# Kernel optimization log

Measured on AMD Instinct MI355X. Metric: run time of the kernel, lower is better.

The kernel has to match this reference:

```python
import jax, jax.numpy as jnp
import numpy as np

VOCAB_SIZE = 256
CODEC_VOCAB = 1024  # 2 ** codec_bits
D = 1024
NHEAD = 16
FF = 4096
L = 6
ENROLLED = 225  # enrolled_codec_sec(3) * codec_rate(75)
B, TT, TA = 4, 128, 512


def sinusoidal_pe(T, d):
    pos = np.arange(T, dtype=np.float32)[:, None]
    div = np.exp(np.arange(0, d, 2, dtype=np.float32) * (-np.log(10000.0) / d))
    pe = np.zeros((T, d), dtype=np.float32)
    pe[:, 0::2] = np.sin(pos * div)
    pe[:, 1::2] = np.cos(pos * div)
    return jnp.asarray(pe)


def layernorm(x, w, b, eps=1e-5):
    mu = x.mean(-1, keepdims=True)
    var = ((x - mu) ** 2).mean(-1, keepdims=True)
    return (x - mu) * jax.lax.rsqrt(var + eps) * w + b


def mha(q_in, kv_in, in_w, in_b, out_w, out_b, mask=None):
    # q_in: [B,Tq,D], kv_in: [B,Tk,D]; mask True == blocked (torch attn_mask convention)
    d = q_in.shape[-1]
    h, hd = NHEAD, d // NHEAD
    wq, wk, wv = in_w[:d], in_w[d:2 * d], in_w[2 * d:]
    bq, bk, bv = in_b[:d], in_b[d:2 * d], in_b[2 * d:]
    Bq, Tq, _ = q_in.shape
    Tk = kv_in.shape[1]
    q = (q_in @ wq.T + bq).reshape(Bq, Tq, h, hd)
    k = (kv_in @ wk.T + bk).reshape(Bq, Tk, h, hd)
    v = (kv_in @ wv.T + bv).reshape(Bq, Tk, h, hd)
    scores = jnp.einsum('bqhd,bkhd->bhqk', q, k) / jnp.sqrt(jnp.float32(hd))
    if mask is not None:
        scores = jnp.where(mask, -jnp.inf, scores)
    attn = jax.nn.softmax(scores, axis=-1)
    o = jnp.einsum('bhqk,bkhd->bqhd', attn, v).reshape(Bq, Tq, d)
    return o @ out_w.T + out_b


def pack(te, ae, ee, tl, al):
    # Ragged concat [text[:tl]; audio[:al]; enrolled] padded to static max_len.
    Tt, Ta, Te = te.shape[0], ae.shape[0], ee.shape[0]
    pos = jnp.arange(Tt + Ta + Te)
    t = te[jnp.clip(pos, 0, Tt - 1)]
    a = ae[jnp.clip(pos - tl, 0, Ta - 1)]
    e = ee[jnp.clip(pos - tl - al, 0, Te - 1)]
    x = jnp.where((pos < tl)[:, None], t,
        jnp.where((pos < tl + al)[:, None], a,
        jnp.where((pos < tl + al + Te)[:, None], e, jnp.zeros_like(t))))
    return x


def setup_inputs():
    key = jax.random.key(0)
    ks = iter(jax.random.split(key, 64))

    def n(shape, s=0.02):
        return jax.random.normal(next(ks), shape, dtype=jnp.float32) * s

    text = jax.random.randint(next(ks), (B, TT), 0, VOCAB_SIZE)
    audio = jax.random.randint(next(ks), (B, TA), 0, CODEC_VOCAB)
    enrolled_audio = jax.random.randint(next(ks), (B, ENROLLED), 0, CODEC_VOCAB)
    # force sample 0 to full length so max_len is static (= TT+TA+ENROLLED)
    text_len_batch = jax.random.randint(next(ks), (B,), TT // 2, TT + 1).at[0].set(TT)
    audio_len_batch = jax.random.randint(next(ks), (B,), TA // 2, TA + 1).at[0].set(TA)
    return dict(
        text=text, audio=audio, enrolled_audio=enrolled_audio,
        text_len_batch=text_len_batch, audio_len_batch=audio_len_batch,
        text_emb=n((VOCAB_SIZE, D)), audio_emb=n((CODEC_VOCAB, D)),
        sa_in_w=n((L, 3 * D, D)), sa_in_b=jnp.zeros((L, 3 * D), jnp.float32),
        sa_out_w=n((L, D, D)), sa_out_b=jnp.zeros((L, D), jnp.float32),
        ca_in_w=n((L, 3 * D, D)), ca_in_b=jnp.zeros((L, 3 * D), jnp.float32),
        ca_out_w=n((L, D, D)), ca_out_b=jnp.zeros((L, D), jnp.float32),
        ff1_w=n((L, FF, D)), ff1_b=jnp.zeros((L, FF), jnp.float32),
        ff2_w=n((L, D, FF)), ff2_b=jnp.zeros((L, D), jnp.float32),
        ln1_w=jnp.ones((L, D), jnp.float32), ln1_b=jnp.zeros((L, D), jnp.float32),
        ln2_w=jnp.ones((L, D), jnp.float32), ln2_b=jnp.zeros((L, D), jnp.float32),
        ln3_w=jnp.ones((L, D), jnp.float32), ln3_b=jnp.zeros((L, D), jnp.float32),
        out_w=n((CODEC_VOCAB, D)), out_b=jnp.zeros((CODEC_VOCAB,), jnp.float32))


def reference(text, audio, enrolled_audio, text_len_batch, audio_len_batch,
              text_emb, audio_emb, sa_in_w, sa_in_b, sa_out_w, sa_out_b,
              ca_in_w, ca_in_b, ca_out_w, ca_out_b, ff1_w, ff1_b, ff2_w, ff2_b,
              ln1_w, ln1_b, ln2_w, ln2_b, ln3_w, ln3_b, out_w, out_b):
    # per-segment sinusoidal PE (positions reset at the start of each segment)
    te = text_emb[text] + sinusoidal_pe(text.shape[1], D)
    ae = audio_emb[audio] + sinusoidal_pe(audio.shape[1], D)
    ee = audio_emb[enrolled_audio] + sinusoidal_pe(enrolled_audio.shape[1], D)
    embed = jax.vmap(pack)(te, ae, ee, text_len_batch, audio_len_batch)  # [B, max_len, D]
    max_len = embed.shape[1]
    prefix = text.shape[1] + audio.shape[1]  # == max(tl+al) by construction
    mask = jnp.triu(jnp.ones((max_len, max_len), bool), 1).at[:, :prefix].set(False)
    mem = embed  # TransformerDecoder memory == embed
    x = embed
    for l in range(L):  # post-norm decoder layers (torch default norm_first=False)
        x = layernorm(x + mha(x, x, sa_in_w[l], sa_in_b[l], sa_out_w[l], sa_out_b[l], mask), ln1_w[l], ln1_b[l])
        x = layernorm(x + mha(x, mem, ca_in_w[l], ca_in_b[l], ca_out_w[l], ca_out_b[l]), ln2_w[l], ln2_b[l])
        h = jax.nn.relu(x @ ff1_w[l].T + ff1_b[l]) @ ff2_w[l].T + ff2_b[l]
        x = layernorm(x + h, ln3_w[l], ln3_b[l])
    return x @ out_w.T + out_b  # [B, max_len, CODEC_VOCAB]
```

## Files before the change

### kernel.cpp

```cpp
#include <hip/hip_runtime.h>
#include <hip/hip_bf16.h>

#define B_      4
#define TT_     128
#define TA_     512
#define TE_     225
#define T_      865
#define D_      1024
#define H_      16
#define FF_     4096
#define L_      6
#define PREFIX_ 640
#define M_TOK   (B_ * T_)
#define M_PAD   3584
#define NKV     (L_ * 2 * D_)

typedef __attribute__((ext_vector_type(8))) short          s16x8;
typedef __attribute__((ext_vector_type(4))) float          f32x4;
typedef __attribute__((ext_vector_type(8))) unsigned short u16x8;

typedef __attribute__((address_space(1))) const void gv_t;
typedef __attribute__((address_space(3))) void       lv_t;

__device__ __forceinline__ float bf2f(unsigned short u) {
  union { unsigned int i; float f; } c; c.i = ((unsigned int)u) << 16; return c.f;
}
__device__ __forceinline__ unsigned short f2bf(float f) {
  union { __hip_bfloat16 h; unsigned short u; } c; c.h = __float2bfloat16(f); return c.u;
}
template <int N> __device__ __forceinline__ void vmwait() {
  asm volatile("s_waitcnt vmcnt(%0)" :: "n"(N) : "memory");
}

__global__ __launch_bounds__(256) void embed_kernel(
    const int* __restrict__ text, const int* __restrict__ audio,
    const int* __restrict__ enrolled, const int* __restrict__ tl_b,
    const int* __restrict__ al_b, const float* __restrict__ text_emb,
    const float* __restrict__ audio_emb,
    float* __restrict__ xf, unsigned short* __restrict__ xb,
    unsigned short* __restrict__ memb, unsigned short* __restrict__ attnb) {
  int row = blockIdx.x;
  int d0 = threadIdx.x * 4;
  size_t off = (size_t)row * D_ + d0;
  if (row >= M_TOK) {
    *(unsigned long long*)&xb[off]    = 0ull;
    *(unsigned long long*)&memb[off]  = 0ull;
    *(unsigned long long*)&attnb[off] = 0ull;
    return;
  }
  int b = row / T_, pos = row - b * T_;
  int tl = tl_b[b], al = al_b[b];
  const float* emb = nullptr;
  int p = 0;
  if (pos < tl) {
    emb = text_emb + (size_t)text[b * TT_ + pos] * D_;
    p = pos;
  } else if (pos < tl + al) {
    emb = audio_emb + (size_t)audio[b * TA_ + (pos - tl)] * D_;
    p = pos - tl;
  } else if (pos < tl + al + TE_) {
    emb = audio_emb + (size_t)enrolled[b * TE_ + (pos - tl - al)] * D_;
    p = pos - tl - al;
  }
  float4 v;
  float* pv = (float*)&v;
  if (emb) {
    const float c = -9.2103403719761836f / (float)D_;
    #pragma unroll
    for (int e = 0; e < 4; ++e) {
      int d = d0 + e;
      int i = d >> 1;
      float freq = expf(c * (float)(2 * i));
      float arg = (float)p * freq;
      float pe = (d & 1) ? cosf(arg) : sinf(arg);
      pv[e] = emb[d] + pe;
    }
  } else {
    v = make_float4(0.f, 0.f, 0.f, 0.f);
  }
  *(float4*)&xf[off] = v;
  unsigned long long pk = (unsigned long long)f2bf(pv[0])
      | ((unsigned long long)f2bf(pv[1]) << 16)
      | ((unsigned long long)f2bf(pv[2]) << 32)
      | ((unsigned long long)f2bf(pv[3]) << 48);
  *(unsigned long long*)&xb[off]   = pk;
  *(unsigned long long*)&memb[off] = pk;
}

__global__ __launch_bounds__(256) void cvt_kernel(
    const float* __restrict__ in, unsigned short* __restrict__ out, int n8) {
  int i = blockIdx.x * 256 + threadIdx.x;
  if (i >= n8) return;
  const float4* pp = (const float4*)in + (size_t)i * 2;
  float4 a = pp[0], bq = pp[1];
  u16x8 o;
  o[0] = f2bf(a.x);  o[1] = f2bf(a.y);  o[2] = f2bf(a.z);  o[3] = f2bf(a.w);
  o[4] = f2bf(bq.x); o[5] = f2bf(bq.y); o[6] = f2bf(bq.z); o[7] = f2bf(bq.w);
  *(u16x8*)(out + (size_t)i * 8) = o;
}

__global__ __launch_bounds__(256) void cvt_layer_kernel(
    const float* __restrict__ s0, const float* __restrict__ s1,
    const float* __restrict__ s2, const float* __restrict__ s3,
    const float* __restrict__ s4, const float* __restrict__ s5,
    unsigned short* __restrict__ dst) {
  size_t e = ((size_t)blockIdx.x * 256 + threadIdx.x) * 8;
  if (e >= 16777216u) return;
  const float* src; size_t off;
  if      (e <  3145728u) { src = s0; off = e; }
  else if (e <  4194304u) { src = s1; off = e -  3145728u; }
  else if (e <  7340032u) { src = s2; off = e -  4194304u; }
  else if (e <  8388608u) { src = s3; off = e -  7340032u; }
  else if (e < 12582912u) { src = s4; off = e -  8388608u; }
  else                    { src = s5; off = e - 12582912u; }
  const float4* pp = (const float4*)(src + off);
  float4 a = pp[0], bq = pp[1];
  u16x8 o;
  o[0] = f2bf(a.x);  o[1] = f2bf(a.y);  o[2] = f2bf(a.z);  o[3] = f2bf(a.w);
  o[4] = f2bf(bq.x); o[5] = f2bf(bq.y); o[6] = f2bf(bq.z); o[7] = f2bf(bq.w);
  *(u16x8*)(dst + e) = o;
}

__global__ __launch_bounds__(256) void cvt_ckv_w(
    const float* __restrict__ ca_in_w, unsigned short* __restrict__ wckv) {
  int rr = blockIdx.x;
  int l = rr / (2 * D_), w = rr % (2 * D_);
  const float* src = ca_in_w + (size_t)l * 3 * D_ * D_ + (size_t)(D_ + w) * D_;
  unsigned short* dst = wckv + (size_t)rr * D_;
  int c = threadIdx.x * 4;
  float4 v4 = *(const float4*)(src + c);
  unsigned long long pk = (unsigned long long)f2bf(v4.x)
      | ((unsigned long long)f2bf(v4.y) << 16)
      | ((unsigned long long)f2bf(v4.z) << 32)
      | ((unsigned long long)f2bf(v4.w) << 48);
  *(unsigned long long*)&dst[c] = pk;
}

__global__ __launch_bounds__(256) void cvt_ckv_b(
    const float* __restrict__ ca_in_b, float* __restrict__ cbias) {
  int rr = blockIdx.x * 256 + threadIdx.x;
  if (rr >= NKV) return;
  int l = rr / (2 * D_), w = rr % (2 * D_);
  cbias[rr] = ca_in_b[(size_t)l * 3 * D_ + D_ + w];
}

template <int ACT, int OBF, int NSTRIPE>
__global__ __launch_bounds__(512, 2) void gemm_8w(
    const unsigned short* __restrict__ A, int lda,
    const unsigned short* __restrict__ W, int ldw,
    const float* __restrict__ bias,
    float* __restrict__ Cf, unsigned short* __restrict__ Cb, int ldc,
    int Mw, int K) {
  __shared__ unsigned short lds[2][2][256 * 64];
  int tid = threadIdx.x, lane = tid & 63, wid = tid >> 6;

  int gx = gridDim.x;
  int nwg = gx * gridDim.y;
  int orig = blockIdx.y * gx + blockIdx.x;
  int m0, n0;
  if (NSTRIPE && (gx & 7) == 0) {
    int stripe = gx >> 3;
    int xcd = orig & 7, loc = orig >> 3;
    n0 = (xcd * stripe + loc % stripe) * 256;
    m0 = (loc / stripe) * 256;
  } else {
    int q = nwg >> 3, r = nwg & 7;
    int xcd = orig & 7, loc = orig >> 3;
    int wg = (xcd < r ? xcd * (q + 1) : r * (q + 1) + (xcd - r) * q) + loc;
    m0 = (wg / gx) * 256;
    n0 = (wg % gx) * 256;
  }

  int wr = wid >> 2, wc = wid & 3;
  int r16 = lane & 15, g4 = lane >> 4;

  int srow = lane >> 3;
  int sgrp = (lane & 7) ^ srow;
  const unsigned short* gA[4];
  const unsigned short* gB[4];
  unsigned soff[4];
  #pragma unroll
  for (int c = 0; c < 4; ++c) {
    int rb = wid * 32 + c * 8;
    gA[c] = A + (size_t)(m0 + rb + srow) * lda + sgrp * 8;
    gB[c] = W + (size_t)(n0 + rb + srow) * ldw + sgrp * 8;
    soff[c] = rb * 64;
  }

  f32x4 acc[8][4];
  #pragma unroll
  for (int i = 0; i < 8; ++i)
    #pragma unroll
    for (int j = 0; j < 4; ++j) acc[i][j] = (f32x4)0.f;

  auto STAGE = [&](int bi, int t) {
    int k0 = t * 64;
    #pragma unroll
    for (int c = 0; c < 4; ++c)
      __builtin_amdgcn_global_load_lds((gv_t*)(gA[c] + k0),
          (lv_t*)&lds[bi][0][soff[c]], 16, 0, 0);
    #pragma unroll
    for (int c = 0; c < 4; ++c)
      __builtin_amdgcn_global_load_lds((gv_t*)(gB[c] + k0),
          (lv_t*)&lds[bi][1][soff[c]], 16, 0, 0);
  };

  STAGE(0, 0);
  int nt = K / 64, cur = 0;
  for (int t = 0; t < nt; ++t) {
    vmwait<0>();
    __builtin_amdgcn_s_barrier();
    if (t + 1 < nt) STAGE(cur ^ 1, t + 1);

    const unsigned short* Ab = &lds[cur][0][0];
    const unsigned short* Bb = &lds[cur][1][0];

    s16x8 bf_[4][2];
    #pragma unroll
    for (int j = 0; j < 4; ++j)
      #pragma unroll
      for (int kk = 0; kk < 2; ++kk) {
        int row = wc * 64 + j * 16 + r16;
        bf_[j][kk] = *(const s16x8*)&Bb[row * 64 + (((kk * 4 + g4) ^ (row & 7)) * 8)];
      }

    #pragma unroll
    for (int p = 0; p < 4; ++p) {
      s16x8 af_[2][2];
      #pragma unroll
      for (int ii = 0; ii < 2; ++ii)
        #pragma unroll
        for (int kk = 0; kk < 2; ++kk) {
          int row = wr * 128 + (p * 2 + ii) * 16 + r16;
          af_[ii][kk] = *(const s16x8*)&Ab[row * 64 + (((kk * 4 + g4) ^ (row & 7)) * 8)];
        }
      __builtin_amdgcn_s_setprio(1);
      #pragma unroll
      for (int kk = 0; kk < 2; ++kk)
        #pragma unroll
        for (int ii = 0; ii < 2; ++ii)
          #pragma unroll
          for (int j = 0; j < 4; ++j)
            acc[p * 2 + ii][j] = __builtin_amdgcn_mfma_f32_16x16x32_bf16(
                af_[ii][kk], bf_[j][kk], acc[p * 2 + ii][j], 0, 0, 0);
      __builtin_amdgcn_s_setprio(0);
    }
    cur ^= 1;
  }

  float bv[4];
  #pragma unroll
  for (int j = 0; j < 4; ++j) bv[j] = bias[n0 + wc * 64 + j * 16 + r16];
  int rbase = m0 + wr * 128 + g4 * 4;
  int cbase = n0 + wc * 64 + r16;
  #pragma unroll
  for (int i = 0; i < 8; ++i)
    #pragma unroll
    for (int rr = 0; rr < 4; ++rr) {
      int m = rbase + i * 16 + rr;
      if (m < Mw) {
        #pragma unroll
        for (int j = 0; j < 4; ++j) {
          float v = acc[i][j][rr] + bv[j];
          if (ACT) v = fmaxf(v, 0.f);
          if (OBF) Cb[(size_t)m * ldc + cbase + j * 16] = f2bf(v);
          else     Cf[(size_t)m * ldc + cbase + j * 16] = v;
        }
      }
    }
}

template <int BM, int BN, int BK, int ACT, int OBF, int NSTRIPE>
__global__ __launch_bounds__(256) void gemm_p2(
    const unsigned short* __restrict__ A, int lda,
    const unsigned short* __restrict__ W, int ldw,
    const float* __restrict__ bias,
    float* __restrict__ Cf, unsigned short* __restrict__ Cb, int ldc,
    int Mw, int K) {
  constexpr int WROWS = BM / 2, WCOLS = BN / 2;
  constexpr int WM = WROWS / 16, WN = WCOLS / 16;
  constexpr int LPR = BK / 8;
  constexpr int RPI = 64 / LPR;
  constexpr int ACH = (BM / 4) / RPI;
  constexpr int BCH = (BN / 4) / RPI;
  constexpr int ABUF = BM * BK, BBUF = BN * BK;
  constexpr int KSUB = BK / 32;
  constexpr int LW = ACH + BCH;
  __shared__ unsigned short lds[3 * (ABUF + BBUF)];

  int tid = threadIdx.x, lane = tid & 63, wid = tid >> 6;
  int gx = gridDim.x;
  int nwg = gx * gridDim.y;
  int orig = blockIdx.y * gx + blockIdx.x;
  int m0, n0;
  if (NSTRIPE && (gx & 7) == 0) {
    int stripe = gx >> 3;
    int xcd = orig & 7, loc = orig >> 3;
    n0 = (xcd * stripe + loc % stripe) * BN;
    m0 = (loc / stripe) * BM;
  } else {
    int q = nwg >> 3, r = nwg & 7;
    int xcd = orig & 7, loc = orig >> 3;
    int wg = (xcd < r ? xcd * (q + 1) : r * (q + 1) + (xcd - r) * q) + loc;
    m0 = (wg / gx) * BM;
    n0 = (wg % gx) * BN;
  }

  int wr = wid >> 1, wc = wid & 1;
  int lrow = lane / LPR, lgrp = lane % LPR;
  int skey = (BK == 32) ? ((lrow >> 1) & 3) : (lrow & 7);
  int lk = (lgrp ^ skey) * 8;

  const unsigned short* gAp[ACH]; unsigned aoff[ACH];
  const unsigned short* gBp[BCH]; unsigned boff[BCH];
  #pragma unroll
  for (int c = 0; c < ACH; ++c) {
    int row0 = wid * (BM / 4) + c * RPI;
    gAp[c] = A + (size_t)(m0 + row0 + lrow) * lda + lk;
    aoff[c] = row0 * BK;
  }
  #pragma unroll
  for (int c = 0; c < BCH; ++c) {
    int row0 = wid * (BN / 4) + c * RPI;
    gBp[c] = W + (size_t)(n0 + row0 + lrow) * ldw + lk;
    boff[c] = row0 * BK;
  }

  f32x4 acc[WM][WN];
  #pragma unroll
  for (int i = 0; i < WM; ++i)
    #pragma unroll
    for (int j = 0; j < WN; ++j) acc[i][j] = (f32x4)0.f;

  int frow = lane & 15, g4 = lane >> 4;

  auto STAGE = [&](int bi, int t) {
    int k0 = t * BK;
    #pragma unroll
    for (int c = 0; c < ACH; ++c)
      __builtin_amdgcn_global_load_lds((gv_t*)(gAp[c] + k0),
          (lv_t*)&lds[bi * ABUF + aoff[c]], 16, 0, 0);
    #pragma unroll
    for (int c = 0; c < BCH; ++c)
      __builtin_amdgcn_global_load_lds((gv_t*)(gBp[c] + k0),
          (lv_t*)&lds[3 * ABUF + bi * BBUF + boff[c]], 16, 0, 0);
  };

  STAGE(0, 0);
  STAGE(1, 1);
  int nt = K / BK;
  int cur = 0;
  for (int t = 0; t < nt; ++t) {
    if (t + 1 < nt) vmwait<LW>(); else vmwait<0>();
    __builtin_amdgcn_s_barrier();
    if (t + 2 < nt) {
      int stb = cur + 2; if (stb >= 3) stb -= 3;
      STAGE(stb, t + 2);
    }
    const unsigned short* Ab = &lds[cur * ABUF];
    const unsigned short* Bb = &lds[3 * ABUF + cur * BBUF];
    #pragma unroll
    for (int kk = 0; kk < KSUB; ++kk) {
      int rk = (BK == 32) ? ((g4 ^ ((frow >> 1) & 3)) * 8)
                          : (((kk * 4 + g4) ^ (frow & 7)) * 8);
      s16x8 af[WM], bfr[WN];
      #pragma unroll
      for (int i = 0; i < WM; ++i)
        af[i] = *(const s16x8*)&Ab[(wr * WROWS + i * 16 + frow) * BK + rk];
      #pragma unroll
      for (int j = 0; j < WN; ++j)
        bfr[j] = *(const s16x8*)&Bb[(wc * WCOLS + j * 16 + frow) * BK + rk];
      __builtin_amdgcn_s_setprio(1);
      #pragma unroll
      for (int i = 0; i < WM; ++i)
        #pragma unroll
        for (int j = 0; j < WN; ++j)
          acc[i][j] = __builtin_amdgcn_mfma_f32_16x16x32_bf16(af[i], bfr[j], acc[i][j], 0, 0, 0);
      __builtin_amdgcn_s_setprio(0);
    }
    cur = (cur == 2) ? 0 : cur + 1;
  }

  float bv[WN];
  #pragma unroll
  for (int j = 0; j < WN; ++j) bv[j] = bias[n0 + wc * WCOLS + j * 16 + (lane & 15)];
  int rbase = m0 + wr * WROWS + (lane >> 4) * 4;
  int cbase = n0 + wc * WCOLS + (lane & 15);
  #pragma unroll
  for (int i = 0; i < WM; ++i)
    #pragma unroll
    for (int rr = 0; rr < 4; ++rr) {
      int m = rbase + i * 16 + rr;
      if (m < Mw) {
        #pragma unroll
        for (int j = 0; j < WN; ++j) {
          float v = acc[i][j][rr] + bv[j];
          if (ACT) v = fmaxf(v, 0.f);
          if (OBF) Cb[(size_t)m * ldc + cbase + j * 16] = f2bf(v);
          else     Cf[(size_t)m * ldc + cbase + j * 16] = v;
        }
      }
    }
}

template <bool MASKED>
__global__ __launch_bounds__(256) void attn_mfma(
    const unsigned short* __restrict__ qp, int qld,
    const unsigned short* __restrict__ kp,
    const unsigned short* __restrict__ vp, int kvld,
    unsigned short* __restrict__ out) {
  __shared__ unsigned short KsL[64 * 64];
  __shared__ unsigned short VtL[64 * 72];
  __shared__ unsigned short PsL[4][16 * 64];
  int tid = threadIdx.x;
  int lane = tid & 63, wid = tid >> 6;
  int b = blockIdx.y >> 4, h = blockIdx.y & 15;
  int q0 = blockIdx.x * 64;
  int r16 = lane & 15, g4 = lane >> 4;

  int qrow = q0 + wid * 16 + r16;
  if (qrow >= T_) qrow = T_ - 1;
  const unsigned short* qbase =
      qp + (size_t)(b * T_ + qrow) * qld + h * 64 + g4 * 8;
  s16x8 qf0 = *(const s16x8*)qbase;
  s16x8 qf1 = *(const s16x8*)(qbase + 32);

  float m_[4], l_[4];
  f32x4 o_[4];
  #pragma unroll
  for (int rg = 0; rg < 4; ++rg) { m_[rg] = -INFINITY; l_[rg] = 0.f; }
  #pragma unroll
  for (int dj = 0; dj < 4; ++dj) o_[dj] = (f32x4)0.f;

  const int nt = MASKED ? max(10, (int)blockIdx.x + 1) : 14;

  for (int t = 0; t < nt; ++t) {
    int k0 = t * 64;
    __syncthreads();

    #pragma unroll
    for (int c = 0; c < 2; ++c) {
      int row = wid * 16 + c * 8 + (lane >> 3);
      int kr = k0 + row; if (kr >= T_) kr = T_ - 1;
      int grp = (lane & 7) ^ (row & 7);
      const unsigned short* src =
          kp + (size_t)(b * T_ + kr) * kvld + h * 64 + grp * 8;
      __builtin_amdgcn_global_load_lds((gv_t*)src,
          (lv_t*)&KsL[(wid * 16 + c * 8) * 64], 16, 0, 0);
    }
    {
      int vkr = k0 + lane; if (vkr >= T_) vkr = T_ - 1;
      const unsigned short* vsrc =
          vp + (size_t)(b * T_ + vkr) * kvld + h * 64 + wid * 16;
      u16x8 v0 = *(const u16x8*)vsrc;
      u16x8 v1 = *(const u16x8*)(vsrc + 8);
      #pragma unroll
      for (int jj = 0; jj < 8; ++jj) {
        VtL[(wid * 16 + jj) * 72 + lane]     = v0[jj];
        VtL[(wid * 16 + 8 + jj) * 72 + lane] = v1[jj];
      }
    }
    __syncthreads();

    f32x4 sj[4];
    #pragma unroll
    for (int j = 0; j < 4; ++j) sj[j] = (f32x4)0.f;
    __builtin_amdgcn_s_setprio(1);
    #pragma unroll
    for (int j = 0; j < 4; ++j) {
      int krow = j * 16 + r16;
      s16x8 kf0 = *(const s16x8*)&KsL[krow * 64 + ((g4 ^ (krow & 7)) * 8)];
      s16x8 kf1 = *(const s16x8*)&KsL[krow * 64 + (((4 + g4) ^ (krow & 7)) * 8)];
      sj[j] = __builtin_amdgcn_mfma_f32_16x16x32_bf16(qf0, kf0, sj[j], 0, 0, 0);
      sj[j] = __builtin_amdgcn_mfma_f32_16x16x32_bf16(qf1, kf1, sj[j], 0, 0, 0);
    }
    __builtin_amdgcn_s_setprio(0);

    float alpha_[4];
    #pragma unroll
    for (int rg = 0; rg < 4; ++rg) {
      int qa = q0 + wid * 16 + g4 * 4 + rg;
      float pm = -INFINITY;
      #pragma unroll
      for (int j = 0; j < 4; ++j) {
        int kg = k0 + j * 16 + r16;
        float sv = sj[j][rg] * 0.125f;
        bool bad = (kg >= T_) || (MASKED && kg > qa && kg >= PREFIX_);
        sv = bad ? -INFINITY : sv;
        sj[j][rg] = sv;
        pm = fmaxf(pm, sv);
      }
      pm = fmaxf(pm, __shfl_xor(pm, 1));
      pm = fmaxf(pm, __shfl_xor(pm, 2));
      pm = fmaxf(pm, __shfl_xor(pm, 4));
      pm = fmaxf(pm, __shfl_xor(pm, 8));
      float mn = fmaxf(m_[rg], pm);
      float al = __expf(m_[rg] - mn);
      m_[rg] = mn;
      alpha_[rg] = al;
      int prow = g4 * 4 + rg;
      float ps = 0.f;
      #pragma unroll
      for (int j = 0; j < 4; ++j) {
        float pv = __expf(sj[j][rg] - mn);
        ps += pv;
        PsL[wid][prow * 64 + (((j * 2 + (r16 >> 3)) ^ (prow & 7)) * 8) + (r16 & 7)]
            = f2bf(pv);
      }
      ps += __shfl_xor(ps, 1);
      ps += __shfl_xor(ps, 2);
      ps += __shfl_xor(ps, 4);
      ps += __shfl_xor(ps, 8);
      l_[rg] = l_[rg] * al + ps;
    }
    #pragma unroll
    for (int dj = 0; dj < 4; ++dj)
      #pragma unroll
      for (int rg = 0; rg < 4; ++rg) o_[dj][rg] *= alpha_[rg];

    __builtin_amdgcn_s_setprio(1);
    #pragma unroll
    for (int kk = 0; kk < 2; ++kk) {
      s16x8 pf = *(const s16x8*)
          &PsL[wid][r16 * 64 + (((kk * 4 + g4) ^ (r16 & 7)) * 8)];
      #pragma unroll
      for (int dj = 0; dj < 4; ++dj) {
        s16x8 vf = *(const s16x8*)
            &VtL[(dj * 16 + r16) * 72 + kk * 32 + g4 * 8];
        o_[dj] = __builtin_amdgcn_mfma_f32_16x16x32_bf16(pf, vf, o_[dj], 0, 0, 0);
      }
    }
    __builtin_amdgcn_s_setprio(0);
  }

  #pragma unroll
  for (int rg = 0; rg < 4; ++rg) {
    int qa = q0 + wid * 16 + g4 * 4 + rg;
    if (qa < T_) {
      float inv = 1.f / l_[rg];
      unsigned short* ob = out + (size_t)(b * T_ + qa) * D_ + h * 64;
      #pragma unroll
      for (int dj = 0; dj < 4; ++dj)
        ob[dj * 16 + r16] = f2bf(o_[dj][rg] * inv);
    }
  }
}

__global__ __launch_bounds__(256) void ln_res_kernel(
    float* __restrict__ x, const float* __restrict__ r,
    const float* __restrict__ w, const float* __restrict__ b,
    unsigned short* __restrict__ xb) {
  __shared__ float red[4];
  int row = blockIdx.x, tid = threadIdx.x;
  size_t off = (size_t)row * D_ + tid * 4;
  float4 xv = *(float4*)&x[off];
  float4 rv = *(const float4*)&r[off];
  float v0 = xv.x + rv.x, v1 = xv.y + rv.y, v2 = xv.z + rv.z, v3 = xv.w + rv.w;

  float s = v0 + v1 + v2 + v3;
  #pragma unroll
  for (int o = 1; o < 64; o <<= 1) s += __shfl_xor(s, o);
  if ((tid & 63) == 0) red[tid >> 6] = s;
  __syncthreads();
  float mu = (red[0] + red[1] + red[2] + red[3]) * (1.f / 1024.f);
  __syncthreads();

  float d0 = v0 - mu, d1 = v1 - mu, d2 = v2 - mu, d3 = v3 - mu;
  float ss = d0 * d0 + d1 * d1 + d2 * d2 + d3 * d3;
  #pragma unroll
  for (int o = 1; o < 64; o <<= 1) ss += __shfl_xor(ss, o);
  if ((tid & 63) == 0) red[tid >> 6] = ss;
  __syncthreads();
  float var = (red[0] + red[1] + red[2] + red[3]) * (1.f / 1024.f);
  float rs = rsqrtf(var + 1e-5f);

  float4 wv = *(const float4*)&w[tid * 4];
  float4 bv = *(const float4*)&b[tid * 4];
  float o0 = d0 * rs * wv.x + bv.x, o1 = d1 * rs * wv.y + bv.y;
  float o2 = d2 * rs * wv.z + bv.z, o3 = d3 * rs * wv.w + bv.w;
  *(float4*)&x[off] = make_float4(o0, o1, o2, o3);
  unsigned long long pk = (unsigned long long)f2bf(o0)
      | ((unsigned long long)f2bf(o1) << 16)
      | ((unsigned long long)f2bf(o2) << 32)
      | ((unsigned long long)f2bf(o3) << 48);
  *(unsigned long long*)&xb[off] = pk;
}

extern "C" void kernel_launch(void* const* d_in, const int* in_sizes, int n_in,
                              void* d_out, int out_size, void* d_ws, size_t ws_size,
                              hipStream_t stream) {
  const int* text       = (const int*)d_in[0];
  const int* audio      = (const int*)d_in[1];
  const int* enrolled   = (const int*)d_in[2];
  const int* tl_b       = (const int*)d_in[3];
  const int* al_b       = (const int*)d_in[4];
  const float* text_emb = (const float*)d_in[5];
  const float* audio_emb= (const float*)d_in[6];
  const float* sa_in_w  = (const float*)d_in[7];
  const float* sa_in_b  = (const float*)d_in[8];
  const float* sa_out_w = (const float*)d_in[9];
  const float* sa_out_b = (const float*)d_in[10];
  const float* ca_in_w  = (const float*)d_in[11];
  const float* ca_in_b  = (const float*)d_in[12];
  const float* ca_out_w = (const float*)d_in[13];
  const float* ca_out_b = (const float*)d_in[14];
  const float* ff1_w    = (const float*)d_in[15];
  const float* ff1_b    = (const float*)d_in[16];
  const float* ff2_w    = (const float*)d_in[17];
  const float* ff2_b    = (const float*)d_in[18];
  const float* ln1_w    = (const float*)d_in[19];
  const float* ln1_b    = (const float*)d_in[20];
  const float* ln2_w    = (const float*)d_in[21];
  const float* ln2_b    = (const float*)d_in[22];
  const float* ln3_w    = (const float*)d_in[23];
  const float* ln3_b    = (const float*)d_in[24];
  const float* out_w    = (const float*)d_in[25];
  const float* out_b    = (const float*)d_in[26];

  char* p = (char*)d_ws;
  float* xf = (float*)p;            p += (size_t)M_PAD * D_ * 4;
  float* tmp = (float*)p;           p += (size_t)M_PAD * D_ * 4;
  unsigned short* xb = (unsigned short*)p;    p += (size_t)M_PAD * D_ * 2;
  unsigned short* memb = (unsigned short*)p;  p += (size_t)M_PAD * D_ * 2;
  unsigned short* qkv = (unsigned short*)p;   p += (size_t)M_PAD * FF_ * 2;
  unsigned short* attnb = (unsigned short*)p; p += (size_t)M_PAD * D_ * 2;
  unsigned short* wbuf = (unsigned short*)p;  p += (size_t)16777216 * 2;
  unsigned short* outwb = (unsigned short*)p; p += (size_t)1048576 * 2;
  unsigned short* ckv  = (unsigned short*)p;  p += (size_t)M_PAD * NKV * 2;
  unsigned short* wckv = (unsigned short*)p;  p += (size_t)NKV * D_ * 2;
  float* cbias = (float*)p;                   p += (size_t)NKV * 4;
  bool fused = ((size_t)(p - (char*)d_ws)) <= ws_size;

  unsigned short* w_sa_qkv = wbuf;
  unsigned short* w_sa_o   = wbuf + 3145728;
  unsigned short* w_ca_qkv = wbuf + 4194304;
  unsigned short* w_ca_o   = wbuf + 7340032;
  unsigned short* w_ff1    = wbuf + 8388608;
  unsigned short* w_ff2    = wbuf + 12582912;

  embed_kernel<<<M_PAD, 256, 0, stream>>>(text, audio, enrolled, tl_b, al_b,
                                          text_emb, audio_emb, xf, xb, memb, attnb);
  cvt_kernel<<<512, 256, 0, stream>>>(out_w, outwb, 131072);

  if (fused) {
    cvt_ckv_w<<<NKV, 256, 0, stream>>>(ca_in_w, wckv);
    cvt_ckv_b<<<NKV / 256, 256, 0, stream>>>(ca_in_b, cbias);
    gemm_8w<0, 1, 1><<<dim3(NKV / 256, M_PAD / 256), 512, 0, stream>>>(
        memb, D_, wckv, D_, cbias, nullptr, ckv, NKV, M_PAD, D_);
  }

  for (int l = 0; l < L_; ++l) {
    const float* sa_in_w_l  = sa_in_w  + (size_t)l * 3 * D_ * D_;
    const float* sa_in_b_l  = sa_in_b  + (size_t)l * 3 * D_;
    const float* sa_out_w_l = sa_out_w + (size_t)l * D_ * D_;
    const float* sa_out_b_l = sa_out_b + (size_t)l * D_;
    const float* ca_in_w_l  = ca_in_w  + (size_t)l * 3 * D_ * D_;
    const float* ca_in_b_l  = ca_in_b  + (size_t)l * 3 * D_;
    const float* ca_out_w_l = ca_out_w + (size_t)l * D_ * D_;
    const float* ca_out_b_l = ca_out_b + (size_t)l * D_;
    const float* ff1_w_l    = ff1_w    + (size_t)l * FF_ * D_;
    const float* ff1_b_l    = ff1_b    + (size_t)l * FF_;
    const float* ff2_w_l    = ff2_w    + (size_t)l * D_ * FF_;
    const float* ff2_b_l    = ff2_b    + (size_t)l * D_;

    cvt_layer_kernel<<<8192, 256, 0, stream>>>(sa_in_w_l, sa_out_w_l, ca_in_w_l,
                                               ca_out_w_l, ff1_w_l, ff2_w_l, wbuf);

    gemm_8w<0, 1, 1><<<dim3(3 * D_ / 256, M_PAD / 256), 512, 0, stream>>>(
        xb, D_, w_sa_qkv, D_, sa_in_b_l, nullptr, qkv, 3 * D_, M_PAD, D_);
    attn_mfma<true><<<dim3(14, B_ * H_), 256, 0, stream>>>(
        qkv, 3 * D_, qkv + D_, qkv + 2 * D_, 3 * D_, attnb);
    gemm_p2<64, 64, 64, 0, 0, 0><<<dim3(D_ / 64, M_PAD / 64), 256, 0, stream>>>(
        attnb, D_, w_sa_o, D_, sa_out_b_l, tmp, nullptr, D_, M_PAD, D_);
    ln_res_kernel<<<M_TOK, 256, 0, stream>>>(xf, tmp, ln1_w + l * D_, ln1_b + l * D_, xb);

    gemm_p2<64, 64, 64, 0, 1, 0><<<dim3(D_ / 64, M_PAD / 64), 256, 0, stream>>>(
        xb, D_, w_ca_qkv, D_, ca_in_b_l, nullptr, qkv, 3 * D_, M_PAD, D_);
    if (fused) {
      attn_mfma<false><<<dim3(14, B_ * H_), 256, 0, stream>>>(
          qkv, 3 * D_, ckv + (size_t)l * 2 * D_, ckv + (size_t)l * 2 * D_ + D_,
          NKV, attnb);
    } else {
      gemm_p2<64, 64, 64, 0, 1, 0><<<dim3(2 * D_ / 64, M_PAD / 64), 256, 0, stream>>>(
          memb, D_, w_ca_qkv + (size_t)D_ * D_, D_, ca_in_b_l + D_,
          nullptr, qkv + D_, 3 * D_, M_PAD, D_);
      attn_mfma<false><<<dim3(14, B_ * H_), 256, 0, stream>>>(
          qkv, 3 * D_, qkv + D_, qkv + 2 * D_, 3 * D_, attnb);
    }
    gemm_p2<64, 64, 64, 0, 0, 0><<<dim3(D_ / 64, M_PAD / 64), 256, 0, stream>>>(
        attnb, D_, w_ca_o, D_, ca_out_b_l, tmp, nullptr, D_, M_PAD, D_);
    ln_res_kernel<<<M_TOK, 256, 0, stream>>>(xf, tmp, ln2_w + l * D_, ln2_b + l * D_, xb);

    gemm_8w<1, 1, 1><<<dim3(FF_ / 256, M_PAD / 256), 512, 0, stream>>>(
        xb, D_, w_ff1, D_, ff1_b_l, nullptr, qkv, FF_, M_PAD, D_);
    gemm_p2<64, 64, 64, 0, 0, 1><<<dim3(D_ / 64, M_PAD / 64), 256, 0, stream>>>(
        qkv, FF_, w_ff2, FF_, ff2_b_l, tmp, nullptr, D_, M_PAD, FF_);
    ln_res_kernel<<<M_TOK, 256, 0, stream>>>(xf, tmp, ln3_w + l * D_, ln3_b + l * D_, xb);
  }

  gemm_p2<64, 64, 64, 0, 0, 0><<<dim3(D_ / 64, M_PAD / 64), 256, 0, stream>>>(
      xb, D_, outwb, D_, out_b, (float*)d_out, nullptr, D_, M_TOK, D_);
}
```

Baseline: 2.112 ms.

## Add 128x128-tile 8-wave GEMM and use it for N=1024 projections

Adds a new GEMM kernel with 128x128 output tiles, 8 waves per block, double-buffered direct global-to-LDS loads with XOR swizzle and XCD-aware block remapping. It replaces the 64x64 gemm_p2 launches for the attention output projections, cross-attention Q projection, FF2 and the final output projection. The larger tiles raise data reuse per block and cut global traffic. The cost is fewer blocks (224 for N=1024), which may underfill the GPU's compute units.

```diff
diff --git a/kernel.cpp b/kernel.cpp
--- a/kernel.cpp
+++ b/kernel.cpp
@@ -261,6 +261,128 @@
       if (m < Mw) {
         #pragma unroll
         for (int j = 0; j < 4; ++j) {
+          float v = acc[i][j][rr] + bv[j];
+          if (ACT) v = fmaxf(v, 0.f);
+          if (OBF) Cb[(size_t)m * ldc + cbase + j * 16] = f2bf(v);
+          else     Cf[(size_t)m * ldc + cbase + j * 16] = v;
+        }
+      }
+    }
+}
+
+template <int ACT, int OBF, int NSTRIPE>
+__global__ __launch_bounds__(512, 2) void gemm_8w128(
+    const unsigned short* __restrict__ A, int lda,
+    const unsigned short* __restrict__ W, int ldw,
+    const float* __restrict__ bias,
+    float* __restrict__ Cf, unsigned short* __restrict__ Cb, int ldc,
+    int Mw, int K) {
+  __shared__ unsigned short lds[2][2][128 * 64];
+  int tid = threadIdx.x, lane = tid & 63, wid = tid >> 6;
+
+  int gx = gridDim.x;
+  int nwg = gx * gridDim.y;
+  int orig = blockIdx.y * gx + blockIdx.x;
+  int m0, n0;
+  if (NSTRIPE && (gx & 7) == 0) {
+    int stripe = gx >> 3;
+    int xcd = orig & 7, loc = orig >> 3;
+    n0 = (xcd * stripe + loc % stripe) * 128;
+    m0 = (loc / stripe) * 128;
+  } else {
+    int q = nwg >> 3, r = nwg & 7;
+    int xcd = orig & 7, loc = orig >> 3;
+    int wg = (xcd < r ? xcd * (q + 1) : r * (q + 1) + (xcd - r) * q) + loc;
+    m0 = (wg / gx) * 128;
+    n0 = (wg % gx) * 128;
+  }
+
+  int wr = wid >> 2, wc = wid & 3;
+  int r16 = lane & 15, g4 = lane >> 4;
+
+  int srow = lane >> 3;
+  int sgrp = (lane & 7) ^ srow;
+  const unsigned short* gA[2];
+  const unsigned short* gB[2];
+  unsigned soff[2];
+  #pragma unroll
+  for (int c = 0; c < 2; ++c) {
+    int rb = wid * 16 + c * 8;
+    gA[c] = A + (size_t)(m0 + rb + srow) * lda + sgrp * 8;
+    gB[c] = W + (size_t)(n0 + rb + srow) * ldw + sgrp * 8;
+    soff[c] = rb * 64;
+  }
+
+  f32x4 acc[4][2];
+  #pragma unroll
+  for (int i = 0; i < 4; ++i)
+    #pragma unroll
+    for (int j = 0; j < 2; ++j) acc[i][j] = (f32x4)0.f;
+
+  auto STAGE = [&](int bi, int t) {
+    int k0 = t * 64;
+    #pragma unroll
+    for (int c = 0; c < 2; ++c)
+      __builtin_amdgcn_global_load_lds((gv_t*)(gA[c] + k0),
+          (lv_t*)&lds[bi][0][soff[c]], 16, 0, 0);
+    #pragma unroll
+    for (int c = 0; c < 2; ++c)
+      __builtin_amdgcn_global_load_lds((gv_t*)(gB[c] + k0),
+          (lv_t*)&lds[bi][1][soff[c]], 16, 0, 0);
+  };
+
+  STAGE(0, 0);
+  int nt = K / 64, cur = 0;
+  for (int t = 0; t < nt; ++t) {
+    vmwait<0>();
+    __builtin_amdgcn_s_barrier();
+    if (t + 1 < nt) STAGE(cur ^ 1, t + 1);
+
+    const unsigned short* Ab = &lds[cur][0][0];
+    const unsigned short* Bb = &lds[cur][1][0];
+
+    s16x8 bf_[2][2];
+    #pragma unroll
+    for (int j = 0; j < 2; ++j)
+      #pragma unroll
+      for (int kk = 0; kk < 2; ++kk) {
+        int row = wc * 32 + j * 16 + r16;
+        bf_[j][kk] = *(const s16x8*)&Bb[row * 64 + (((kk * 4 + g4) ^ (row & 7)) * 8)];
+      }
+    s16x8 af_[4][2];
+    #pragma unroll
+    for (int ii = 0; ii < 4; ++ii)
+      #pragma unroll
+      for (int kk = 0; kk < 2; ++kk) {
+        int row = wr * 64 + ii * 16 + r16;
+        af_[ii][kk] = *(const s16x8*)&Ab[row * 64 + (((kk * 4 + g4) ^ (row & 7)) * 8)];
+      }
+    __builtin_amdgcn_s_setprio(1);
+    #pragma unroll
+    for (int kk = 0; kk < 2; ++kk)
+      #pragma unroll
+      for (int ii = 0; ii < 4; ++ii)
+        #pragma unroll
+        for (int j = 0; j < 2; ++j)
+          acc[ii][j] = __builtin_amdgcn_mfma_f32_16x16x32_bf16(
+              af_[ii][kk], bf_[j][kk], acc[ii][j], 0, 0, 0);
+    __builtin_amdgcn_s_setprio(0);
+    cur ^= 1;
+  }
+
+  float bv[2];
+  #pragma unroll
+  for (int j = 0; j < 2; ++j) bv[j] = bias[n0 + wc * 32 + j * 16 + r16];
+  int rbase = m0 + wr * 64 + g4 * 4;
+  int cbase = n0 + wc * 32 + r16;
+  #pragma unroll
+  for (int i = 0; i < 4; ++i)
+    #pragma unroll
+    for (int rr = 0; rr < 4; ++rr) {
+      int m = rbase + i * 16 + rr;
+      if (m < Mw) {
+        #pragma unroll
+        for (int j = 0; j < 2; ++j) {
           float v = acc[i][j][rr] + bv[j];
           if (ACT) v = fmaxf(v, 0.f);
           if (OBF) Cb[(size_t)m * ldc + cbase + j * 16] = f2bf(v);
@@ -670,11 +792,11 @@
         xb, D_, w_sa_qkv, D_, sa_in_b_l, nullptr, qkv, 3 * D_, M_PAD, D_);
     attn_mfma<true><<<dim3(14, B_ * H_), 256, 0, stream>>>(
         qkv, 3 * D_, qkv + D_, qkv + 2 * D_, 3 * D_, attnb);
-    gemm_p2<64, 64, 64, 0, 0, 0><<<dim3(D_ / 64, M_PAD / 64), 256, 0, stream>>>(
+    gemm_8w128<0, 0, 0><<<dim3(D_ / 128, M_PAD / 128), 512, 0, stream>>>(
         attnb, D_, w_sa_o, D_, sa_out_b_l, tmp, nullptr, D_, M_PAD, D_);
     ln_res_kernel<<<M_TOK, 256, 0, stream>>>(xf, tmp, ln1_w + l * D_, ln1_b + l * D_, xb);
 
-    gemm_p2<64, 64, 64, 0, 1, 0><<<dim3(D_ / 64, M_PAD / 64), 256, 0, stream>>>(
+    gemm_8w128<0, 1, 0><<<dim3(D_ / 128, M_PAD / 128), 512, 0, stream>>>(
         xb, D_, w_ca_qkv, D_, ca_in_b_l, nullptr, qkv, 3 * D_, M_PAD, D_);
     if (fused) {
       attn_mfma<false><<<dim3(14, B_ * H_), 256, 0, stream>>>(
@@ -687,17 +809,17 @@
       attn_mfma<false><<<dim3(14, B_ * H_), 256, 0, stream>>>(
           qkv, 3 * D_, qkv + D_, qkv + 2 * D_, 3 * D_, attnb);
     }
-    gemm_p2<64, 64, 64, 0, 0, 0><<<dim3(D_ / 64, M_PAD / 64), 256, 0, stream>>>(
+    gemm_8w128<0, 0, 0><<<dim3(D_ / 128, M_PAD / 128), 512, 0, stream>>>(
         attnb, D_, w_ca_o, D_, ca_out_b_l, tmp, nullptr, D_, M_PAD, D_);
     ln_res_kernel<<<M_TOK, 256, 0, stream>>>(xf, tmp, ln2_w + l * D_, ln2_b + l * D_, xb);
 
     gemm_8w<1, 1, 1><<<dim3(FF_ / 256, M_PAD / 256), 512, 0, stream>>>(
         xb, D_, w_ff1, D_, ff1_b_l, nullptr, qkv, FF_, M_PAD, D_);
-    gemm_p2<64, 64, 64, 0, 0, 1><<<dim3(D_ / 64, M_PAD / 64), 256, 0, stream>>>(
+    gemm_8w128<0, 0, 1><<<dim3(D_ / 128, M_PAD / 128), 512, 0, stream>>>(
         qkv, FF_, w_ff2, FF_, ff2_b_l, tmp, nullptr, D_, M_PAD, FF_);
     ln_res_kernel<<<M_TOK, 256, 0, stream>>>(xf, tmp, ln3_w + l * D_, ln3_b + l * D_, xb);
   }
 
-  gemm_p2<64, 64, 64, 0, 0, 0><<<dim3(D_ / 64, M_PAD / 64), 256, 0, stream>>>(
+  gemm_8w128<0, 0, 0><<<dim3(D_ / 128, M_PAD / 128), 512, 0, stream>>>(
       xb, D_, outwb, D_, out_b, (float*)d_out, nullptr, D_, M_TOK, D_);
 }
```

Measured after the change: 2.047 ms. 1.03x faster.
